# Kernel tuning notes

Measured on AMD Instinct MI355X. Metric: run time of the kernel, lower is better.

Reference implementation:

```python
import jax, jax.numpy as jnp
import numpy as np

DROPOUT_P = 0.2
DROPOUT_KEY = 42  # fixed key: deterministic dropout for the correctness baseline


def setup_inputs() -> dict:
    key = jax.random.key(0)
    kq, kk = jax.random.split(key)
    B, T, D = 4, 1024, 64
    # uniform[0,1): positive so log() in the original is finite (0 maps to -inf,
    # but exp(log q + log k) still yields q*k == 0, consistent with the math)
    q = jax.random.uniform(kq, (B, T, D), dtype=jnp.float32)
    k = jax.random.uniform(kk, (B, T, D), dtype=jnp.float32)
    return {"q": q, "k": k, "T": T, "block_size": T}


def reference(q, k, T, block_size):
    # exp(log(q)_i + log(k)_j) summed over d == sum_d q_id * k_jd == q @ k^T
    # (mathematically identical for the positive inputs the module requires);
    # expressed as a matmul to avoid the (B,T,T,d) blowup while keeping the same math.
    scale = k.shape[-1] ** (-0.5)
    scores = jnp.einsum('bqd,bkd->bqk', q, k) * scale  # (B,T,T)
    causal = jnp.tril(jnp.ones((block_size, block_size), dtype=bool))[:T, :T]
    scores = jnp.where(causal, scores, -jnp.inf)
    probs = jax.nn.softmax(scores, axis=-1)
    # dropout (training mode in original), deterministic key for reproducibility
    keep = jax.random.bernoulli(jax.random.key(DROPOUT_KEY), 1.0 - DROPOUT_P, probs.shape)
    return jnp.where(keep, probs / (1.0 - DROPOUT_P), 0.0)
```

## Files before the change

### kernel.cpp

```cpp
#include <hip/hip_runtime.h>
#include <stdint.h>

#define TT 1024
#define BB 4

typedef __fp16 fp16x2 __attribute__((ext_vector_type(2)));
typedef __fp16 fp16x8 __attribute__((ext_vector_type(8)));
typedef float  floatx4 __attribute__((ext_vector_type(4)));
union U32H2 { uint32_t u; fp16x2 h; };
union U4H8  { uint4 u; fp16x8 h; };

__device__ __forceinline__ uint32_t rotl32(uint32_t x, int d) {
  return (x << d) | (x >> (32 - d));
}

__device__ __forceinline__ bool keep_at(uint32_t i) {
  uint32_t x0 = 0u, x1 = i;
  const uint32_t ks0 = 0u, ks1 = 42u;
  const uint32_t ks2 = 0x1BD11BDAu ^ ks0 ^ ks1;
  x0 += ks0; x1 += ks1;
#define R4(a,b,c,d)                              \
  x0 += x1; x1 = rotl32(x1,(a)); x1 ^= x0;       \
  x0 += x1; x1 = rotl32(x1,(b)); x1 ^= x0;       \
  x0 += x1; x1 = rotl32(x1,(c)); x1 ^= x0;       \
  x0 += x1; x1 = rotl32(x1,(d)); x1 ^= x0;
  R4(13,15,26,6)   x0 += ks1; x1 += ks2 + 1u;
  R4(17,29,16,24)  x0 += ks2; x1 += ks0 + 2u;
  R4(13,15,26,6)   x0 += ks0; x1 += ks1 + 3u;
  R4(17,29,16,24)  x0 += ks1; x1 += ks2 + 4u;
  R4(13,15,26,6)   x0 += ks2; x1 += ks0 + 5u;
#undef R4
  const uint32_t bits = x0 ^ x1;
  const float u = __uint_as_float((bits >> 9) | 0x3f800000u) - 1.0f;
  return u < 0.8f;
}

__device__ __forceinline__ uint32_t pack2(float x, float y) {
  U32H2 t; t.h = __builtin_amdgcn_cvt_pkrtz(x, y);
  return t.u;
}
__device__ __forceinline__ U4H8 pack8(float4 f0, float4 f1) {
  U4H8 d;
  d.u.x = pack2(f0.x, f0.y); d.u.y = pack2(f0.z, f0.w);
  d.u.z = pack2(f1.x, f1.y); d.u.w = pack2(f1.z, f1.w);
  return d;
}

template <int CTRL>
__device__ __forceinline__ float adddpp(float x) {
  const int s =
      __builtin_amdgcn_update_dpp(0, __float_as_int(x), CTRL, 0xF, 0xF, true);
  return x + __int_as_float(s);
}
__device__ __forceinline__ float radd16(float a) {
  a = adddpp<0xB1>(a);  a = adddpp<0x4E>(a);
  a = adddpp<0x141>(a); a = adddpp<0x140>(a);
  return a;
}

__global__ __launch_bounds__(256)
void score_kernel(const float* __restrict__ Q, const float* __restrict__ K,
                  _Float16* __restrict__ E, float* __restrict__ SP) {
  __shared__ float redS[16][4];

  const int tid  = threadIdx.x;
  const int wv   = tid >> 6, ln = tid & 63;
  const int colL = ln & 15;
  const int kgrp = ln >> 4;
  const int cc   = blockIdx.x & 3;
  const int g    = (blockIdx.x >> 2) & 63;
  const int b    = blockIdx.x >> 8;

  const float4* Qf = reinterpret_cast<const float4*>(Q) + (size_t)b * TT * 16;
  const float4* Kf = reinterpret_cast<const float4*>(K) + (size_t)b * TT * 16;

  const int arow = g + 64 * (ln & 15);
  const U4H8 qa0 = pack8(Qf[arow * 16 + kgrp * 2],     Qf[arow * 16 + kgrp * 2 + 1]);
  const U4H8 qa1 = pack8(Qf[arow * 16 + 8 + kgrp * 2], Qf[arow * 16 + 8 + kgrp * 2 + 1]);

  int rowD[4]; uint32_t obase[4];
#pragma unroll
  for (int r = 0; r < 4; ++r) {
    rowD[r]  = g + 64 * (kgrp * 4 + r);
    obase[r] = ((uint32_t)b << 20) | ((uint32_t)rowD[r] << 10);
  }

  float sAcc[4] = {0.f, 0.f, 0.f, 0.f};
#pragma unroll
  for (int it = 0; it < 4; ++it) {
    const int jt = cc * 16 + it * 4 + wv;
    const int jrow = jt * 16 + colL;
    const U4H8 kb0 = pack8(Kf[jrow * 16 + kgrp * 2],
                           Kf[jrow * 16 + kgrp * 2 + 1]);
    const U4H8 kb1 = pack8(Kf[jrow * 16 + 8 + kgrp * 2],
                           Kf[jrow * 16 + 8 + kgrp * 2 + 1]);
    floatx4 acc = {0.f, 0.f, 0.f, 0.f};
    acc = __builtin_amdgcn_mfma_f32_16x16x32_f16(qa0.h, kb0.h, acc, 0, 0, 0);
    acc = __builtin_amdgcn_mfma_f32_16x16x32_f16(qa1.h, kb1.h, acc, 0, 0, 0);
    const int col = jt * 16 + colL;
#pragma unroll
    for (int r = 0; r < 4; ++r) {
      if (g + 64 * (12 + r) >= jt * 16) {
        const float e = (col <= rowD[r]) ? __expf(acc[r] * 0.125f) : 0.f;
        sAcc[r] += e;
        E[obase[r] + (uint32_t)col] = (_Float16)e;
      }
    }
  }
#pragma unroll
  for (int r = 0; r < 4; ++r) sAcc[r] = radd16(sAcc[r]);
  if (colL == 0) {
#pragma unroll
    for (int r = 0; r < 4; ++r) redS[kgrp * 4 + r][wv] = sAcc[r];
  }
  __syncthreads();
  if (wv == 0 && colL == 0) {
#pragma unroll
    for (int r = 0; r < 4; ++r) {
      const int m = kgrp * 4 + r;
      const float S = redS[m][0] + redS[m][1] + redS[m][2] + redS[m][3];
      SP[(((b << 10) + g + 64 * m) << 2) + cc] = S;
    }
  }
}

__global__ __launch_bounds__(256)
void drop_kernel(const _Float16* __restrict__ E, const float* __restrict__ SP,
                 float* __restrict__ O) {
  const int gb  = blockIdx.x;
  const int row = gb & 1023;
  const int tid = threadIdx.x;
  const uint32_t base = (uint32_t)gb << 10;
  const float4 sp = reinterpret_cast<const float4*>(SP)[gb];
  const float rs = 1.25f / (sp.x + sp.y + sp.z + sp.w);
  const int col0 = tid * 4;

  float4 v = {0.f, 0.f, 0.f, 0.f};
  if ((tid & ~63) * 4 <= row) {
    const fp16x2* E2 = reinterpret_cast<const fp16x2*>(E + base + col0);
    const fp16x2 e01 = E2[0], e23 = E2[1];
    const uint32_t i0 = base + (uint32_t)col0;
    if (col0 + 0 <= row) v.x = keep_at(i0 + 0) ? (float)e01[0] * rs : 0.f;
    if (col0 + 1 <= row) v.y = keep_at(i0 + 1) ? (float)e01[1] * rs : 0.f;
    if (col0 + 2 <= row) v.z = keep_at(i0 + 2) ? (float)e23[0] * rs : 0.f;
    if (col0 + 3 <= row) v.w = keep_at(i0 + 3) ? (float)e23[1] * rs : 0.f;
  }
  *reinterpret_cast<float4*>(O + base + col0) = v;
}

extern "C" void kernel_launch(void* const* d_in, const int* in_sizes, int n_in,
                              void* d_out, int out_size, void* d_ws, size_t ws_size,
                              hipStream_t stream) {
  const float* q = (const float*)d_in[0];
  const float* k = (const float*)d_in[1];
  float* out = (float*)d_out;
  _Float16* E = (_Float16*)d_ws;
  float* SP = (float*)((char*)d_ws + (size_t)BB * TT * TT * 2);
  score_kernel<<<dim3(BB * 64 * 4), 256, 0, stream>>>(q, k, E, SP);
  drop_kernel<<<dim3(BB * TT), 256, 0, stream>>>(E, SP, out);
}
```

Measured before the change: 27.11 us.

## Precompute fp16 MFMA-ordered Q/K fragments in a separate conversion kernel

Adds a small kernel that converts Q and K to fp16 once and writes them in the exact per-lane MFMA fragment order, so the score kernel loads one coalesced uint4 per fragment instead of strided float4 pairs and repeated per-block conversions. It also replaces the float-based dropout threshold with a direct integer comparison on the Philox output. The trade-off is an extra kernel launch and a round trip through the workspace.

```diff
diff --git a/kernel.cpp b/kernel.cpp
--- a/kernel.cpp
+++ b/kernel.cpp
@@ -30,20 +30,12 @@
   R4(17,29,16,24)  x0 += ks1; x1 += ks2 + 4u;
   R4(13,15,26,6)   x0 += ks2; x1 += ks0 + 5u;
 #undef R4
-  const uint32_t bits = x0 ^ x1;
-  const float u = __uint_as_float((bits >> 9) | 0x3f800000u) - 1.0f;
-  return u < 0.8f;
+  return (x0 ^ x1) < 3435974144u;
 }
 
 __device__ __forceinline__ uint32_t pack2(float x, float y) {
   U32H2 t; t.h = __builtin_amdgcn_cvt_pkrtz(x, y);
   return t.u;
-}
-__device__ __forceinline__ U4H8 pack8(float4 f0, float4 f1) {
-  U4H8 d;
-  d.u.x = pack2(f0.x, f0.y); d.u.y = pack2(f0.z, f0.w);
-  d.u.z = pack2(f1.x, f1.y); d.u.w = pack2(f1.z, f1.w);
-  return d;
 }
 
 template <int CTRL>
@@ -59,8 +51,26 @@
 }
 
 __global__ __launch_bounds__(256)
-void score_kernel(const float* __restrict__ Q, const float* __restrict__ K,
-                  _Float16* __restrict__ E, float* __restrict__ SP) {
+void cvt_kernel(const float* __restrict__ Q, const float* __restrict__ K,
+                uint32_t* __restrict__ W) {
+  const int t = blockIdx.x * 256 + threadIdx.x;
+  uint4* W4 = reinterpret_cast<uint4*>(W);
+  const bool isK = t >= 32768;
+  const int t2 = t & 32767;
+  const int ln = t2 & 63, c = (t2 >> 6) & 1, tile = (t2 >> 7) & 63, b = t2 >> 13;
+  const int row = tile * (isK ? 16 : 1) + (isK ? (ln & 15) : 64 * (ln & 15));
+  const float4* src = reinterpret_cast<const float4*>(isK ? K : Q) +
+                      ((size_t)(b << 10) + row) * 16 + c * 8 + (ln >> 4) * 2;
+  const float4 f0 = src[0], f1 = src[1];
+  uint4 d;
+  d.x = pack2(f0.x, f0.y); d.y = pack2(f0.z, f0.w);
+  d.z = pack2(f1.x, f1.y); d.w = pack2(f1.z, f1.w);
+  W4[t] = d;
+}
+
+__global__ __launch_bounds__(256)
+void score_kernel(const uint32_t* __restrict__ W, _Float16* __restrict__ E,
+                  float* __restrict__ SP) {
   __shared__ float redS[16][4];
 
   const int tid  = threadIdx.x;
@@ -71,12 +81,13 @@
   const int g    = (blockIdx.x >> 2) & 63;
   const int b    = blockIdx.x >> 8;
 
-  const float4* Qf = reinterpret_cast<const float4*>(Q) + (size_t)b * TT * 16;
-  const float4* Kf = reinterpret_cast<const float4*>(K) + (size_t)b * TT * 16;
+  const uint4* W4 = reinterpret_cast<const uint4*>(W);
+  const uint4* Qp = W4 + (size_t)b * 8192;
+  const uint4* Kp = W4 + 32768 + (size_t)b * 8192;
 
-  const int arow = g + 64 * (ln & 15);
-  const U4H8 qa0 = pack8(Qf[arow * 16 + kgrp * 2],     Qf[arow * 16 + kgrp * 2 + 1]);
-  const U4H8 qa1 = pack8(Qf[arow * 16 + 8 + kgrp * 2], Qf[arow * 16 + 8 + kgrp * 2 + 1]);
+  U4H8 qa0, qa1;
+  qa0.u = Qp[(g * 2 + 0) * 64 + ln];
+  qa1.u = Qp[(g * 2 + 1) * 64 + ln];
 
   int rowD[4]; uint32_t obase[4];
 #pragma unroll
@@ -89,11 +100,9 @@
 #pragma unroll
   for (int it = 0; it < 4; ++it) {
     const int jt = cc * 16 + it * 4 + wv;
-    const int jrow = jt * 16 + colL;
-    const U4H8 kb0 = pack8(Kf[jrow * 16 + kgrp * 2],
-                           Kf[jrow * 16 + kgrp * 2 + 1]);
-    const U4H8 kb1 = pack8(Kf[jrow * 16 + 8 + kgrp * 2],
-                           Kf[jrow * 16 + 8 + kgrp * 2 + 1]);
+    U4H8 kb0, kb1;
+    kb0.u = Kp[(jt * 2 + 0) * 64 + ln];
+    kb1.u = Kp[(jt * 2 + 1) * 64 + ln];
     floatx4 acc = {0.f, 0.f, 0.f, 0.f};
     acc = __builtin_amdgcn_mfma_f32_16x16x32_f16(qa0.h, kb0.h, acc, 0, 0, 0);
     acc = __builtin_amdgcn_mfma_f32_16x16x32_f16(qa1.h, kb1.h, acc, 0, 0, 0);
@@ -154,8 +163,10 @@
   const float* q = (const float*)d_in[0];
   const float* k = (const float*)d_in[1];
   float* out = (float*)d_out;
-  _Float16* E = (_Float16*)d_ws;
-  float* SP = (float*)((char*)d_ws + (size_t)BB * TT * TT * 2);
-  score_kernel<<<dim3(BB * 64 * 4), 256, 0, stream>>>(q, k, E, SP);
+  uint32_t* w = (uint32_t*)d_ws;
+  _Float16* E = (_Float16*)((char*)d_ws + (1 << 20));
+  float* SP = (float*)((char*)d_ws + (1 << 20) + (size_t)BB * TT * TT * 2);
+  cvt_kernel<<<dim3(256), 256, 0, stream>>>(q, k, w);
+  score_kernel<<<dim3(BB * 64 * 4), 256, 0, stream>>>(w, E, SP);
   drop_kernel<<<dim3(BB * TT), 256, 0, stream>>>(E, SP, out);
 }
```

After: 25.17 us. -7.2%, faster.
